# Optimization experiments

Measured on AMD Instinct MI355X. Metric: run time of the kernel, lower is better.

## Reference

```python
import jax, jax.numpy as jnp
import numpy as np

B, T, HW, N, HID, K, OUT = 8, 64, 64, 64, 64, 2, 1
DT = 0.1


def setup_inputs() -> dict:
    key = jax.random.key(0)
    ks = jax.random.split(key, 16)
    nrm = lambda k, shape, s: jax.random.normal(k, shape, jnp.float32) * s
    return {
        "frames": jax.random.uniform(ks[0], (B, T, HW, HW, 3), jnp.float32),
        "adjacency": jax.random.uniform(ks[1], (B, T, N, N), jnp.float32) / N,
        "hidden0": jnp.zeros((B, N, HID), jnp.float32),
        "Wc1": nrm(ks[2], (32, 3, 3, 3), 0.3), "bc1": jnp.zeros(32, jnp.float32),
        "Wc2": nrm(ks[3], (64, 32, 3, 3), 0.08), "bc2": jnp.zeros(64, jnp.float32),
        "Wc3": nrm(ks[4], (128, 64, 3, 3), 0.06), "bc3": jnp.zeros(128, jnp.float32),
        "We": nrm(ks[5], (128, HID), 0.09), "be": jnp.zeros(HID, jnp.float32),
        "Wh": nrm(ks[6], (K + 1, HID, HID), 0.12),
        "Wx": nrm(ks[7], (K + 1, HID, HID), 0.12),
        "bg": jnp.zeros(HID, jnp.float32),
        "tau": jnp.ones(HID, jnp.float32),
        "Ap": nrm(ks[8], (HID,), 1.0),
        "Wd1": nrm(ks[9], (HID, 128), 0.12), "bd1": jnp.zeros(128, jnp.float32),
        "Wd2": nrm(ks[10], (128, 64), 0.09), "bd2": jnp.zeros(64, jnp.float32),
        "Wd3": nrm(ks[11], (64, OUT), 0.12), "bd3": jnp.zeros(OUT, jnp.float32),
    }


def _conv_relu(x, w, b, stride):
    # torch Conv2d(k=3, stride=2, padding=1) == explicit padding (1,1)
    y = jax.lax.conv_general_dilated(
        x, w, (stride, stride), [(1, 1), (1, 1)],
        dimension_numbers=("NCHW", "OIHW", "NCHW"))
    return jax.nn.relu(y + b[None, :, None, None])


def _forward(frames, adjacency, hidden0, Wc1, bc1, Wc2, bc2, Wc3, bc3,
             We, be, Wh, Wx, bg, tau, Ap, Wd1, bd1, Wd2, bd2, Wd3, bd3):
    Bn, Tn, Hh, Ww, C = frames.shape
    # faithful to torch .view(-1, C, H, W): raw memory reinterpretation
    x = frames.reshape(Bn * Tn, C, Hh, Ww)
    x = _conv_relu(x, Wc1, bc1, 2)   # [BT,32,32,32]
    x = _conv_relu(x, Wc2, bc2, 2)   # [BT,64,16,16]
    x = _conv_relu(x, Wc3, bc3, 2)   # [BT,128,8,8]; AdaptiveAvgPool2d((8,8)) is identity here
    feats = x.reshape(Bn, Tn, 128, 8, 8).transpose(0, 1, 3, 4, 2).reshape(Bn, Tn, 64, 128)
    node = feats @ We + be           # [B,T,N,HID]

    Kp = Wh.shape[0] - 1
    eye = jnp.eye(adjacency.shape[-1], dtype=frames.dtype)

    def step(h, inputs):
        xt, At = inputs              # [B,N,HID], [B,N,N]
        powers = [jnp.broadcast_to(eye, At.shape)]
        p = At
        for _ in range(Kp):          # static K-loop -> [I, A, ..., A^K]
            powers.append(p)
            p = jnp.matmul(p, At)
        S = jnp.stack(powers)        # [K+1,B,N,N]
        z = jnp.einsum("bnd,kde->kbne", h, Wh) + jnp.einsum("bnd,kde->kbne", xt, Wx)
        gc = jnp.einsum("kbnm,kbme->bne", S, z) + bg
        f = jnp.tanh(gc)
        h_next = h + DT * (-(1.0 / tau + f) * h + f * Ap)  # liquid time-constant Euler step
        m = h_next.mean(axis=1)      # [B,HID]
        d = jax.nn.relu(m @ Wd1 + bd1)
        d = jax.nn.relu(d @ Wd2 + bd2)
        c = d @ Wd3 + bd3            # [B,OUT]
        return h_next, c

    xs = (node.transpose(1, 0, 2, 3), adjacency.transpose(1, 0, 2, 3))
    final_h, controls = jax.lax.scan(step, hidden0, xs)
    controls = controls.transpose(1, 0, 2)  # [B,T,OUT]
    return controls, final_h


def reference(frames, adjacency, hidden0, Wc1, bc1, Wc2, bc2, Wc3, bc3,
              We, be, Wh, Wx, bg, tau, Ap, Wd1, bd1, Wd2, bd2, Wd3, bd3):
    return _forward(frames, adjacency, hidden0, Wc1, bc1, Wc2, bc2, Wc3, bc3,
                    We, be, Wh, Wx, bg, tau, Ap, Wd1, bd1, Wd2, bd2, Wd3, bd3)
```

## Files before the change

### kernel.cpp

```cpp
#include <hip/hip_runtime.h>
#include <hip/hip_bf16.h>

#define SH 68
#define DT_C 0.1f

typedef short bfrag __attribute__((ext_vector_type(8)));
typedef _Float16 hfrag __attribute__((ext_vector_type(8)));
typedef float f32x4 __attribute__((ext_vector_type(4)));

union FU { bfrag v; unsigned short s[8]; uint4 q; };
union HU { hfrag v; unsigned short s[8]; uint4 q; };

__device__ __forceinline__ unsigned short bf16_rn(float x) {
  union { float f; unsigned u; } v; v.f = x;
  unsigned r = v.u + 0x7fffu + ((v.u >> 16) & 1u);
  return (unsigned short)(r >> 16);
}
__device__ __forceinline__ float bf16_tof(unsigned short h) {
  union { unsigned u; float f; } v; v.u = ((unsigned)h) << 16; return v.f;
}
__device__ __forceinline__ unsigned short bfu(float x) {
  union { __hip_bfloat16 b; unsigned short u; } cv;
  cv.b = __float2bfloat16(x);
  return cv.u;
}
__device__ __forceinline__ float tanh_f(float x) {
  return 1.0f - 2.0f / (__expf(2.0f * x) + 1.0f);
}
__device__ __forceinline__ void h16split(float v, unsigned short& hu, unsigned short& lu) {
  union { _Float16 h; unsigned short u; } a, b;
  a.h = (_Float16)v;
  b.h = (_Float16)(v - (float)a.h);
  hu = a.u; lu = b.u;
}
__device__ __forceinline__ unsigned short h16hi(float v) {
  union { _Float16 h; unsigned short u; } a; a.h = (_Float16)v; return a.u;
}

__device__ __forceinline__ void mm16(const float* __restrict__ A,
                                     const float* __restrict__ B, int sb,
                                     float acc[4][4], int n0, int e0) {
  #pragma unroll 4
  for (int k4 = 0; k4 < 16; ++k4) {
    float4 av0 = *(const float4*)(A + (n0+0)*SH + k4*4);
    float4 av1 = *(const float4*)(A + (n0+1)*SH + k4*4);
    float4 av2 = *(const float4*)(A + (n0+2)*SH + k4*4);
    float4 av3 = *(const float4*)(A + (n0+3)*SH + k4*4);
    const float a0j[4] = {av0.x, av0.y, av0.z, av0.w};
    const float a1j[4] = {av1.x, av1.y, av1.z, av1.w};
    const float a2j[4] = {av2.x, av2.y, av2.z, av2.w};
    const float a3j[4] = {av3.x, av3.y, av3.z, av3.w};
    #pragma unroll
    for (int j = 0; j < 4; ++j) {
      const float4 bv = *(const float4*)(B + (k4*4+j)*sb + e0);
      acc[0][0]+=a0j[j]*bv.x; acc[0][1]+=a0j[j]*bv.y; acc[0][2]+=a0j[j]*bv.z; acc[0][3]+=a0j[j]*bv.w;
      acc[1][0]+=a1j[j]*bv.x; acc[1][1]+=a1j[j]*bv.y; acc[1][2]+=a1j[j]*bv.z; acc[1][3]+=a1j[j]*bv.w;
      acc[2][0]+=a2j[j]*bv.x; acc[2][1]+=a2j[j]*bv.y; acc[2][2]+=a2j[j]*bv.z; acc[2][3]+=a2j[j]*bv.w;
      acc[3][0]+=a3j[j]*bv.x; acc[3][1]+=a3j[j]*bv.y; acc[3][2]+=a3j[j]*bv.z; acc[3][3]+=a3j[j]*bv.w;
    }
  }
}

__global__ __launch_bounds__(256) void wprep_k(const float* __restrict__ Wc2,
                                               const float* __restrict__ Wc3,
                                               const float* __restrict__ Wh,
                                               const float* __restrict__ We,
                                               unsigned short* __restrict__ W2h,
                                               unsigned short* __restrict__ W2l,
                                               unsigned short* __restrict__ W3h,
                                               unsigned short* __restrict__ W3l,
                                               unsigned short* __restrict__ WTh,
                                               unsigned short* __restrict__ WTl,
                                               unsigned short* __restrict__ WeTh,
                                               unsigned short* __restrict__ WeTl) {
  int i = blockIdx.x * 256 + threadIdx.x;
  if (i < 18432) {
    int oc = i / 288, rem = i % 288, pos = rem >> 5, ic = rem & 31;
    float v = Wc2[oc*288 + ic*9 + pos];
    h16split(v, W2h[i], W2l[i]);
  } else if (i < 18432 + 73728) {
    int j = i - 18432;
    int oc = j / 576, rem = j % 576, pos = rem >> 6, ic = rem & 63;
    float v = Wc3[oc*576 + ic*9 + pos];
    h16split(v, W3h[j], W3l[j]);
  } else if (i < 18432 + 73728 + 12288) {
    int j = i - 92160;
    int k3 = j >> 12, rem = j & 4095, din = rem >> 6, dout = rem & 63;
    float v = Wh[j];
    unsigned short hi = bf16_rn(v);
    WTh[k3*4096 + dout*64 + din] = hi;
    WTl[k3*4096 + dout*64 + din] = bf16_rn(v - bf16_tof(hi));
  } else if (i < 18432 + 73728 + 12288 + 8192) {
    int j = i - 104448;
    int e = j >> 7, oc = j & 127;
    float v = We[oc*64 + e];
    h16split(v, WeTh[j], WeTl[j]);
  }
}

__global__ __launch_bounds__(256) void conv1_k(const float* __restrict__ frames,
                                               const float* __restrict__ W,
                                               const float* __restrict__ bias,
                                               unsigned short* __restrict__ c1h) {
  __shared__ __align__(16) float sIn[12288];
  int bt = blockIdx.x, tid = threadIdx.x;
  const float4* src = (const float4*)(frames + (size_t)bt * 12288);
  for (int i = tid; i < 3072; i += 256) ((float4*)sIn)[i] = src[i];
  __syncthreads();
  for (int p = tid; p < 1024; p += 256) {
    int ho = p >> 5, wo = p & 31, hi0 = ho*2-1, wi0 = wo*2-1;
    int obase = (((ho*2 + (wo&1))*16 + (wo>>1)))*8;
    for (int ocb = 0; ocb < 4; ++ocb) {
      float acc[8];
      #pragma unroll
      for (int j = 0; j < 8; ++j) acc[j] = bias[ocb*8+j];
      for (int ic = 0; ic < 3; ++ic) {
        float win[9];
        #pragma unroll
        for (int kh = 0; kh < 3; ++kh) {
          int hi = hi0 + kh;
          #pragma unroll
          for (int kw = 0; kw < 3; ++kw) {
            int wi = wi0 + kw;
            win[kh*3+kw] = (hi>=0 && hi<64 && wi>=0 && wi<64) ? sIn[ic*4096 + hi*64 + wi] : 0.f;
          }
        }
        #pragma unroll
        for (int j = 0; j < 8; ++j) {
          const float* wp = W + (size_t)(ocb*8+j)*27 + ic*9;
          #pragma unroll
          for (int k = 0; k < 9; ++k) acc[j] += win[k] * wp[k];
        }
      }
      ushort hh[8];
      #pragma unroll
      for (int j = 0; j < 8; ++j) hh[j] = h16hi(fmaxf(acc[j], 0.f));
      *(uint4*)&c1h[(size_t)bt*32768 + ocb*8192 + obase] = *(uint4*)hh;
    }
  }
}

#define MFMAH(a, bb, cc) __builtin_amdgcn_mfma_f32_16x16x32_f16((a), (bb), (cc), 0, 0, 0)

__global__ __launch_bounds__(256) void conv2m_k(const unsigned short* __restrict__ c1h,
                                                const unsigned short* __restrict__ W2h,
                                                const unsigned short* __restrict__ W2l,
                                                const float* __restrict__ bias,
                                                unsigned short* __restrict__ c2h) {
  __shared__ __align__(16) unsigned short sH[32768];
  int bt = blockIdx.x, tid = threadIdx.x;
  {
    const uint4* gh = (const uint4*)(c1h + (size_t)bt*32768);
    for (int i = tid; i < 4096; i += 256) ((uint4*)sH)[i] = gh[i];
  }
  __syncthreads();
  int lane = tid & 63, w = tid >> 6, g = lane >> 4, c = lane & 15;
  f32x4 acc[4][4] = {};
  const uint4 z4 = make_uint4(0,0,0,0);
  #pragma unroll
  for (int pos = 0; pos < 9; ++pos) {
    const int kh = pos / 3, kw = pos % 3;
    HU Ah[4];
    #pragma unroll
    for (int m = 0; m < 4; ++m) {
      int pix = w*64 + m*16 + c;
      int ho = pix >> 4, wo = pix & 15;
      int hi = 2*ho - 1 + kh, wi = 2*wo - 1 + kw;
      bool ok = (hi >= 0) & (wi >= 0);
      int hic = ok ? hi : 0, wic = ok ? wi : 0;
      int a = (((g*32 + hic)*2 + (wic & 1))*16 + (wic >> 1))*8;
      uint4 vh = *(const uint4*)&sH[a];
      Ah[m].q = ok ? vh : z4;
    }
    HU Bh[4], Bl[4];
    #pragma unroll
    for (int n = 0; n < 4; ++n) {
      int off = (n*16 + c)*288 + pos*32 + g*8;
      Bh[n].q = *(const uint4*)(W2h + off);
      Bl[n].q = *(const uint4*)(W2l + off);
    }
    #pragma unroll
    for (int m = 0; m < 4; ++m)
      #pragma unroll
      for (int n = 0; n < 4; ++n) {
        acc[m][n] = MFMAH(Ah[m].v, Bh[n].v, acc[m][n]);
        acc[m][n] = MFMAH(Ah[m].v, Bl[n].v, acc[m][n]);
      }
  }
  #pragma unroll
  for (int n = 0; n < 4; ++n) {
    int oc = n*16 + c;
    float bv = bias[oc];
    int ks3 = oc >> 3, il = oc & 7;
    #pragma unroll
    for (int m = 0; m < 4; ++m) {
      #pragma unroll
      for (int r = 0; r < 4; ++r) {
        int pix = w*64 + m*16 + 4*g + r;
        int ho = pix >> 4, wo = pix & 15;
        float v = fmaxf(acc[m][n][r] + bv, 0.f);
        size_t dst = (size_t)bt*16384 + ((((ks3*16 + ho)*2 + (wo&1))*8 + (wo>>1)))*8 + il;
        c2h[dst] = h16hi(v);
      }
    }
  }
}

__global__ __launch_bounds__(256) void conv3e_k(const unsigned short* __restrict__ c2h,
                                                const unsigned short* __restrict__ W3h,
                                                const unsigned short* __restrict__ W3l,
                                                const float* __restrict__ bias,
                                                const unsigned short* __restrict__ WeTh,
                                                const unsigned short* __restrict__ WeTl,
                                                const float* __restrict__ be,
                                                float* __restrict__ node) {
  __shared__ __align__(16) unsigned short sH[16384];
  __shared__ __align__(16) unsigned short sF[64*136];
  int bt = blockIdx.x, tid = threadIdx.x;
  {
    const uint4* gh = (const uint4*)(c2h + (size_t)bt*16384);
    for (int i = tid; i < 2048; i += 256) ((uint4*)sH)[i] = gh[i];
  }
  __syncthreads();
  int lane = tid & 63, w = tid >> 6, g = lane >> 4, c = lane & 15;
  f32x4 acc[8] = {};
  const uint4 z4 = make_uint4(0,0,0,0);
  int pix = w*16 + c;
  int ho = pix >> 3, wo = pix & 7;
  #pragma unroll
  for (int pos = 0; pos < 9; ++pos) {
    const int kh = pos / 3, kw = pos % 3;
    int hi = 2*ho - 1 + kh, wi = 2*wo - 1 + kw;
    bool ok = (hi >= 0) & (wi >= 0);
    int hic = ok ? hi : 0, wic = ok ? wi : 0;
    #pragma unroll
    for (int ih = 0; ih < 2; ++ih) {
      int icg = ih*4 + g;
      int a = ((((icg*16 + hic)*2 + (wic & 1))*8 + (wic >> 1)))*8;
      HU Ah;
      uint4 vh = *(const uint4*)&sH[a];
      Ah.q = ok ? vh : z4;
      #pragma unroll
      for (int n = 0; n < 8; ++n) {
        int off = (n*16 + c)*576 + pos*64 + ih*32 + g*8;
        HU Bh, Bl;
        Bh.q = *(const uint4*)(W3h + off);
        Bl.q = *(const uint4*)(W3l + off);
        acc[n] = MFMAH(Ah.v, Bh.v, acc[n]);
        acc[n] = MFMAH(Ah.v, Bl.v, acc[n]);
      }
    }
  }
  #pragma unroll
  for (int n = 0; n < 8; ++n) {
    int oc = n*16 + c;
    float bv = bias[oc];
    #pragma unroll
    for (int r = 0; r < 4; ++r) {
      int po = w*16 + 4*g + r;
      sF[po*136 + oc] = h16hi(fmaxf(acc[n][r] + bv, 0.f));
    }
  }
  __syncthreads();
  f32x4 eacc[4] = {{0.f,0.f,0.f,0.f},{0.f,0.f,0.f,0.f},{0.f,0.f,0.f,0.f},{0.f,0.f,0.f,0.f}};
  #pragma unroll
  for (int kt = 0; kt < 4; ++kt) {
    HU Af;
    Af.q = *(const uint4*)&sF[(w*16 + c)*136 + kt*32 + g*8];
    #pragma unroll
    for (int n = 0; n < 4; ++n) {
      int off = (n*16 + c)*128 + kt*32 + g*8;
      HU Bh, Bl;
      Bh.q = *(const uint4*)(WeTh + off);
      Bl.q = *(const uint4*)(WeTl + off);
      eacc[n] = MFMAH(Af.v, Bh.v, eacc[n]);
      eacc[n] = MFMAH(Af.v, Bl.v, eacc[n]);
    }
  }
  #pragma unroll
  for (int n = 0; n < 4; ++n) {
    int e = n*16 + c;
    float bev = be[e];
    #pragma unroll
    for (int r = 0; r < 4; ++r) {
      int po = w*16 + 4*g + r;
      node[(size_t)bt*4096 + po*64 + e] = eacc[n][r] + bev;
    }
  }
}

__global__ __launch_bounds__(256) void prep_k(const float* __restrict__ adj,
                                              const float* __restrict__ node,
                                              const float* __restrict__ Wx,
                                              unsigned short* __restrict__ Abf,
                                              unsigned short* __restrict__ A2bf,
                                              float* __restrict__ gxg) {
  __shared__ __align__(16) float sA[64*SH], sA2[64*SH], sN[64*SH], sZ[64*SH];
  int bt = blockIdx.x, tid = threadIdx.x;
  {
    const float4* a4 = (const float4*)(adj + (size_t)bt * 4096);
    const float4* n4 = (const float4*)(node + (size_t)bt * 4096);
    for (int i = tid; i < 1024; i += 256) {
      int r = i >> 4, c = (i & 15) * 4;
      *(float4*)&sA[r*SH+c] = a4[i];
      *(float4*)&sN[r*SH+c] = n4[i];
    }
  }
  __syncthreads();
  int lane = tid & 63, w = tid >> 6, nsub = lane >> 4, eb = lane & 15;
  int n0 = w*16 + nsub*4, e0 = eb*4;
  float4* gxout = (float4*)(gxg + (size_t)bt * 4096);
  for (int i = tid; i < 1024; i += 256) {
    int r = i >> 4, c0 = (i & 15) * 4;
    ushort4 o;
    o.x = bf16_rn(sA[r*SH+c0+0]); o.y = bf16_rn(sA[r*SH+c0+1]);
    o.z = bf16_rn(sA[r*SH+c0+2]); o.w = bf16_rn(sA[r*SH+c0+3]);
    *(ushort4*)&Abf[(size_t)bt*4096 + r*64 + c0] = o;
  }
  {
    float a2t[4][4] = {};
    mm16(sA, sA, SH, a2t, n0, e0);
    #pragma unroll
    for (int jj = 0; jj < 4; ++jj) {
      *(float4*)&sA2[(n0+jj)*SH+e0] = make_float4(a2t[jj][0], a2t[jj][1], a2t[jj][2], a2t[jj][3]);
      ushort4 o;
      o.x = bf16_rn(a2t[jj][0]); o.y = bf16_rn(a2t[jj][1]);
      o.z = bf16_rn(a2t[jj][2]); o.w = bf16_rn(a2t[jj][3]);
      *(ushort4*)&A2bf[(size_t)bt*4096 + (n0+jj)*64 + e0] = o;
    }
  }
  {
    float t[4][4] = {};
    mm16(sN, Wx + 4096, 64, t, n0, e0);
    #pragma unroll
    for (int jj = 0; jj < 4; ++jj)
      *(float4*)&sZ[(n0+jj)*SH+e0] = make_float4(t[jj][0], t[jj][1], t[jj][2], t[jj][3]);
  }
  __syncthreads();
  float gx[4][4] = {};
  mm16(sA, sZ, SH, gx, n0, e0);
  __syncthreads();
  {
    float t[4][4] = {};
    mm16(sN, Wx + 8192, 64, t, n0, e0);
    #pragma unroll
    for (int jj = 0; jj < 4; ++jj)
      *(float4*)&sZ[(n0+jj)*SH+e0] = make_float4(t[jj][0], t[jj][1], t[jj][2], t[jj][3]);
  }
  __syncthreads();
  mm16(sA2, sZ, SH, gx, n0, e0);
  mm16(sN, Wx, 64, gx, n0, e0);
  #pragma unroll
  for (int jj = 0; jj < 4; ++jj)
    gxout[(n0+jj)*16 + eb] = make_float4(gx[jj][0], gx[jj][1], gx[jj][2], gx[jj][3]);
}

#define MFMA(a, bb, cc) __builtin_amdgcn_mfma_f32_16x16x32_bf16((a), (bb), (cc), 0, 0, 0)

__global__ __launch_bounds__(1024, 4) void seq2_k(
    const unsigned short* __restrict__ Abf, const unsigned short* __restrict__ A2bf,
    const float* __restrict__ gxg, const float* __restrict__ h0,
    const unsigned short* __restrict__ WTh, const unsigned short* __restrict__ WTl,
    const float* __restrict__ bg, const float* __restrict__ tau, const float* __restrict__ Apv,
    float* __restrict__ mout, float* __restrict__ out) {
  __shared__ unsigned short sHh[64*72];
  __shared__ unsigned short sA[2][64*72], sA2[2][64*72];
  __shared__ unsigned short sZ1[64*72], sZ2[64*72];
  __shared__ float sPart[64*17];
  int b = blockIdx.x, tid = threadIdx.x;
  int lane = tid & 63, w = tid >> 6, g = lane >> 4, c = lane & 15;
  int mt = w & 3, nt = w >> 2;
  int e = nt*16 + c;
  int mrow = mt*16 + 4*g;
  float itau = 1.f/tau[e], apv = Apv[e], bgv = bg[e];
  FU wf[3][2][2];
  #pragma unroll
  for (int k3 = 0; k3 < 3; ++k3)
    #pragma unroll
    for (int kt = 0; kt < 2; ++kt) {
      int off = k3*4096 + e*64 + kt*32 + 8*g;
      wf[k3][kt][0].q = *(const uint4*)(WTh + off);
      wf[k3][kt][1].q = *(const uint4*)(WTl + off);
    }
  float hm[4];
  #pragma unroll
  for (int r = 0; r < 4; ++r) hm[r] = h0[(size_t)b*4096 + (mrow+r)*64 + e];
  #pragma unroll
  for (int r = 0; r < 4; ++r) sHh[(mrow+r)*72 + e] = bfu(hm[r]);
  {
    int row = tid >> 4, k0 = (tid & 15) * 4;
    *(uint2*)&sA[0][row*72 + k0]  = *(const uint2*)(Abf  + (size_t)b*64*4096 + tid*4);
    *(uint2*)&sA2[0][row*72 + k0] = *(const uint2*)(A2bf + (size_t)b*64*4096 + tid*4);
  }
  __syncthreads();
  #pragma unroll 1
  for (int t = 0; t < 64; ++t) {
    int cur = t & 1;
    size_t bt = (size_t)b*64 + t;
    int tn = (t < 63) ? t + 1 : t;
    uint2 pa  = *(const uint2*)(Abf  + ((size_t)b*64 + tn)*4096 + tid*4);
    uint2 pa2 = *(const uint2*)(A2bf + ((size_t)b*64 + tn)*4096 + tid*4);
    float gxv[4];
    {
      const float* gp = gxg + bt*4096;
      #pragma unroll
      for (int r = 0; r < 4; ++r) gxv[r] = gp[(mrow+r)*64 + e];
    }
    FU ha[2];
    #pragma unroll
    for (int kt = 0; kt < 2; ++kt)
      ha[kt].q = *(const uint4*)&sHh[(mt*16 + c)*72 + kt*32 + 8*g];
    f32x4 a1 = {0.f,0.f,0.f,0.f}, a2 = {0.f,0.f,0.f,0.f};
    #pragma unroll
    for (int kt = 0; kt < 2; ++kt) {
      a1 = MFMA(ha[kt].v, wf[1][kt][0].v, a1);
      a1 = MFMA(ha[kt].v, wf[1][kt][1].v, a1);
      a2 = MFMA(ha[kt].v, wf[2][kt][0].v, a2);
      a2 = MFMA(ha[kt].v, wf[2][kt][1].v, a2);
    }
    {
      ushort4 o1, o2;
      o1.x = bfu(a1[0]); o1.y = bfu(a1[1]); o1.z = bfu(a1[2]); o1.w = bfu(a1[3]);
      o2.x = bfu(a2[0]); o2.y = bfu(a2[1]); o2.z = bfu(a2[2]); o2.w = bfu(a2[3]);
      *(ushort4*)&sZ1[e*72 + mrow] = o1;
      *(ushort4*)&sZ2[e*72 + mrow] = o2;
    }
    __syncthreads();
    f32x4 acc = {0.f,0.f,0.f,0.f};
    #pragma unroll
    for (int kt = 0; kt < 2; ++kt) {
      FU aA, aA2, z1f, z2f;
      int ao = (mt*16 + c)*72 + kt*32 + 8*g;
      aA.q  = *(const uint4*)&sA[cur][ao];
      aA2.q = *(const uint4*)&sA2[cur][ao];
      z1f.q = *(const uint4*)&sZ1[e*72 + kt*32 + 8*g];
      z2f.q = *(const uint4*)&sZ2[e*72 + kt*32 + 8*g];
      acc = MFMA(ha[kt].v, wf[0][kt][0].v, acc);
      acc = MFMA(ha[kt].v, wf[0][kt][1].v, acc);
      acc = MFMA(aA.v,  z1f.v, acc);
      acc = MFMA(aA2.v, z2f.v, acc);
    }
    float ps = 0.f;
    #pragma unroll
    for (int r = 0; r < 4; ++r) {
      float gc = acc[r] + gxv[r] + bgv;
      float f = tanh_f(gc);
      float hn = hm[r] + DT_C * (-(itau + f) * hm[r] + f * apv);
      hm[r] = hn;
      ps += hn;
      sHh[(mrow+r)*72 + e] = bfu(hn);
    }
    sPart[e*17 + mt*4 + g] = ps;
    {
      int row = tid >> 4, k0 = (tid & 15) * 4;
      *(uint2*)&sA[cur^1][row*72 + k0]  = pa;
      *(uint2*)&sA2[cur^1][row*72 + k0] = pa2;
    }
    __syncthreads();
    if (lane < 4) {
      int ee = w*4 + lane;
      float s = 0.f;
      #pragma unroll
      for (int j = 0; j < 16; ++j) s += sPart[ee*17 + j];
      mout[bt*64 + ee] = s * (1.0f / 64.0f);
    }
  }
  #pragma unroll
  for (int r = 0; r < 4; ++r)
    out[512 + (size_t)b*4096 + (mrow+r)*64 + e] = hm[r];
}

__global__ __launch_bounds__(128) void dec_k(const float* __restrict__ mout,
                                             const float* __restrict__ Wd1, const float* __restrict__ bd1,
                                             const float* __restrict__ Wd2, const float* __restrict__ bd2,
                                             const float* __restrict__ Wd3, const float* __restrict__ bd3,
                                             float* __restrict__ out) {
  __shared__ float sm[64], sd1[128], sd2[64];
  int bt = blockIdx.x, tid = threadIdx.x;
  if (tid < 64) sm[tid] = mout[(size_t)bt*64 + tid];
  __syncthreads();
  {
    float a = bd1[tid];
    #pragma unroll 8
    for (int e = 0; e < 64; ++e) a += sm[e] * Wd1[e*128 + tid];
    sd1[tid] = fmaxf(a, 0.f);
  }
  __syncthreads();
  if (tid < 64) {
    float a = bd2[tid];
    #pragma unroll 8
    for (int i = 0; i < 128; ++i) a += sd1[i] * Wd2[i*64 + tid];
    sd2[tid] = fmaxf(a, 0.f);
  }
  __syncthreads();
  if (tid < 64) {
    float p = sd2[tid] * Wd3[tid];
    #pragma unroll
    for (int off = 32; off > 0; off >>= 1) p += __shfl_down(p, off, 64);
    if (tid == 0) out[bt] = p + bd3[0];
  }
}

extern "C" void kernel_launch(void* const* d_in, const int* in_sizes, int n_in,
                              void* d_out, int out_size, void* d_ws, size_t ws_size,
                              hipStream_t stream) {
  const float* frames = (const float*)d_in[0];
  const float* adj    = (const float*)d_in[1];
  const float* h0     = (const float*)d_in[2];
  const float* Wc1 = (const float*)d_in[3];  const float* bc1 = (const float*)d_in[4];
  const float* Wc2 = (const float*)d_in[5];  const float* bc2 = (const float*)d_in[6];
  const float* Wc3 = (const float*)d_in[7];  const float* bc3 = (const float*)d_in[8];
  const float* We  = (const float*)d_in[9];  const float* be  = (const float*)d_in[10];
  const float* Wh  = (const float*)d_in[11]; const float* Wx  = (const float*)d_in[12];
  const float* bg  = (const float*)d_in[13]; const float* tau = (const float*)d_in[14];
  const float* Ap  = (const float*)d_in[15];
  const float* Wd1 = (const float*)d_in[16]; const float* bd1 = (const float*)d_in[17];
  const float* Wd2 = (const float*)d_in[18]; const float* bd2 = (const float*)d_in[19];
  const float* Wd3 = (const float*)d_in[20]; const float* bd3 = (const float*)d_in[21];

  float* ws = (float*)d_ws;
  unsigned short* c1h = (unsigned short*)(ws);
  unsigned short* c2h = (unsigned short*)(ws + 16777216);
  unsigned short* W2h = (unsigned short*)(ws + 20971520);
  unsigned short* W2l = (unsigned short*)(ws + 20980736);
  unsigned short* W3h = (unsigned short*)(ws + 20989952);
  unsigned short* W3l = (unsigned short*)(ws + 21026816);
  unsigned short* WTh = (unsigned short*)(ws + 21063680);
  unsigned short* WTl = (unsigned short*)(ws + 21069824);
  unsigned short* WeTh = (unsigned short*)(ws + 21075968);
  unsigned short* WeTl = (unsigned short*)(ws + 21080064);
  float* node = ws + 4194304;
  float* gx   = ws + 6291456;
  unsigned short* Abf  = (unsigned short*)(ws + 8388608);
  unsigned short* A2bf = (unsigned short*)(ws + 9437184);
  float* mo   = ws + 10485760;
  float* out  = (float*)d_out;

  wprep_k <<<440, 256, 0, stream>>>(Wc2, Wc3, Wh, We, W2h, W2l, W3h, W3l, WTh, WTl, WeTh, WeTl);
  conv1_k <<<512, 256, 0, stream>>>(frames, Wc1, bc1, c1h);
  conv2m_k<<<512, 256, 0, stream>>>(c1h, W2h, W2l, bc2, c2h);
  conv3e_k<<<512, 256, 0, stream>>>(c2h, W3h, W3l, bc3, WeTh, WeTl, be, node);
  prep_k  <<<512, 256, 0, stream>>>(adj, node, Wx, Abf, A2bf, gx);
  seq2_k  <<<8,  1024, 0, stream>>>(Abf, A2bf, gx, h0, WTh, WTl, bg, tau, Ap, mo, out);
  dec_k   <<<512, 128, 0, stream>>>(mo, Wd1, bd1, Wd2, bd2, Wd3, bd3, out);
}
```

Before: 302.2 us.

## Move adjacency-precompute kernel from FP32 FMA to split-bf16 MFMA

Replaces the scalar FP32 prep kernel (A^2, node@Wx terms, and gx accumulation) with an MFMA-based version that splits operands into bf16 hi/lo pairs and uses three MFMAs per product to keep near-FP32 accuracy. Wx is pre-transposed and split in the weight-prep kernel, and the block grows to 512 threads. This targets the per-timestep prep cost that runs before the sequential scan, in exchange for extra split/convert work and more shared-memory traffic.

After: 293.4 us. 1.03x faster.

```diff
diff --git a/kernel.cpp b/kernel.cpp
--- a/kernel.cpp
+++ b/kernel.cpp
@@ -1,8 +1,8 @@
 #include <hip/hip_runtime.h>
 #include <hip/hip_bf16.h>
 
-#define SH 68
 #define DT_C 0.1f
+#define PS 72
 
 typedef short bfrag __attribute__((ext_vector_type(8)));
 typedef _Float16 hfrag __attribute__((ext_vector_type(8)));
@@ -37,34 +37,11 @@
   union { _Float16 h; unsigned short u; } a; a.h = (_Float16)v; return a.u;
 }
 
-__device__ __forceinline__ void mm16(const float* __restrict__ A,
-                                     const float* __restrict__ B, int sb,
-                                     float acc[4][4], int n0, int e0) {
-  #pragma unroll 4
-  for (int k4 = 0; k4 < 16; ++k4) {
-    float4 av0 = *(const float4*)(A + (n0+0)*SH + k4*4);
-    float4 av1 = *(const float4*)(A + (n0+1)*SH + k4*4);
-    float4 av2 = *(const float4*)(A + (n0+2)*SH + k4*4);
-    float4 av3 = *(const float4*)(A + (n0+3)*SH + k4*4);
-    const float a0j[4] = {av0.x, av0.y, av0.z, av0.w};
-    const float a1j[4] = {av1.x, av1.y, av1.z, av1.w};
-    const float a2j[4] = {av2.x, av2.y, av2.z, av2.w};
-    const float a3j[4] = {av3.x, av3.y, av3.z, av3.w};
-    #pragma unroll
-    for (int j = 0; j < 4; ++j) {
-      const float4 bv = *(const float4*)(B + (k4*4+j)*sb + e0);
-      acc[0][0]+=a0j[j]*bv.x; acc[0][1]+=a0j[j]*bv.y; acc[0][2]+=a0j[j]*bv.z; acc[0][3]+=a0j[j]*bv.w;
-      acc[1][0]+=a1j[j]*bv.x; acc[1][1]+=a1j[j]*bv.y; acc[1][2]+=a1j[j]*bv.z; acc[1][3]+=a1j[j]*bv.w;
-      acc[2][0]+=a2j[j]*bv.x; acc[2][1]+=a2j[j]*bv.y; acc[2][2]+=a2j[j]*bv.z; acc[2][3]+=a2j[j]*bv.w;
-      acc[3][0]+=a3j[j]*bv.x; acc[3][1]+=a3j[j]*bv.y; acc[3][2]+=a3j[j]*bv.z; acc[3][3]+=a3j[j]*bv.w;
-    }
-  }
-}
-
 __global__ __launch_bounds__(256) void wprep_k(const float* __restrict__ Wc2,
                                                const float* __restrict__ Wc3,
                                                const float* __restrict__ Wh,
                                                const float* __restrict__ We,
+                                               const float* __restrict__ Wx,
                                                unsigned short* __restrict__ W2h,
                                                unsigned short* __restrict__ W2l,
                                                unsigned short* __restrict__ W3h,
@@ -72,29 +49,38 @@
                                                unsigned short* __restrict__ WTh,
                                                unsigned short* __restrict__ WTl,
                                                unsigned short* __restrict__ WeTh,
-                                               unsigned short* __restrict__ WeTl) {
+                                               unsigned short* __restrict__ WeTl,
+                                               unsigned short* __restrict__ WxTh,
+                                               unsigned short* __restrict__ WxTl) {
   int i = blockIdx.x * 256 + threadIdx.x;
   if (i < 18432) {
     int oc = i / 288, rem = i % 288, pos = rem >> 5, ic = rem & 31;
     float v = Wc2[oc*288 + ic*9 + pos];
     h16split(v, W2h[i], W2l[i]);
-  } else if (i < 18432 + 73728) {
+  } else if (i < 92160) {
     int j = i - 18432;
     int oc = j / 576, rem = j % 576, pos = rem >> 6, ic = rem & 63;
     float v = Wc3[oc*576 + ic*9 + pos];
     h16split(v, W3h[j], W3l[j]);
-  } else if (i < 18432 + 73728 + 12288) {
+  } else if (i < 104448) {
     int j = i - 92160;
     int k3 = j >> 12, rem = j & 4095, din = rem >> 6, dout = rem & 63;
     float v = Wh[j];
     unsigned short hi = bf16_rn(v);
     WTh[k3*4096 + dout*64 + din] = hi;
     WTl[k3*4096 + dout*64 + din] = bf16_rn(v - bf16_tof(hi));
-  } else if (i < 18432 + 73728 + 12288 + 8192) {
+  } else if (i < 112640) {
     int j = i - 104448;
     int e = j >> 7, oc = j & 127;
     float v = We[oc*64 + e];
     h16split(v, WeTh[j], WeTl[j]);
+  } else if (i < 124928) {
+    int j = i - 112640;
+    int k3 = j >> 12, rem = j & 4095, e = rem >> 6, din = rem & 63;
+    float v = Wx[k3*4096 + din*64 + e];
+    unsigned short hi = bf16_rn(v);
+    WxTh[j] = hi;
+    WxTl[j] = bf16_rn(v - bf16_tof(hi));
   }
 }
 
@@ -289,73 +275,172 @@
   }
 }
 
-__global__ __launch_bounds__(256) void prep_k(const float* __restrict__ adj,
-                                              const float* __restrict__ node,
-                                              const float* __restrict__ Wx,
-                                              unsigned short* __restrict__ Abf,
-                                              unsigned short* __restrict__ A2bf,
-                                              float* __restrict__ gxg) {
-  __shared__ __align__(16) float sA[64*SH], sA2[64*SH], sN[64*SH], sZ[64*SH];
+#define MFMA(a, bb, cc) __builtin_amdgcn_mfma_f32_16x16x32_bf16((a), (bb), (cc), 0, 0, 0)
+
+__global__ __launch_bounds__(512) void prepm_k(const float* __restrict__ adj,
+                                               const float* __restrict__ node,
+                                               const unsigned short* __restrict__ WxTh,
+                                               const unsigned short* __restrict__ WxTl,
+                                               unsigned short* __restrict__ Abf,
+                                               unsigned short* __restrict__ A2bf,
+                                               float* __restrict__ gxg) {
+  __shared__ __align__(16) unsigned short sAh[64*PS], sAl[64*PS];
+  __shared__ __align__(16) unsigned short sXh[64*PS], sXl[64*PS];
+  __shared__ __align__(16) unsigned short sNh[64*PS], sNl[64*PS];
+  __shared__ __align__(16) unsigned short sZh[64*PS], sZl[64*PS];
   int bt = blockIdx.x, tid = threadIdx.x;
-  {
-    const float4* a4 = (const float4*)(adj + (size_t)bt * 4096);
-    const float4* n4 = (const float4*)(node + (size_t)bt * 4096);
-    for (int i = tid; i < 1024; i += 256) {
-      int r = i >> 4, c = (i & 15) * 4;
-      *(float4*)&sA[r*SH+c] = a4[i];
-      *(float4*)&sN[r*SH+c] = n4[i];
-    }
-  }
-  __syncthreads();
-  int lane = tid & 63, w = tid >> 6, nsub = lane >> 4, eb = lane & 15;
-  int n0 = w*16 + nsub*4, e0 = eb*4;
-  float4* gxout = (float4*)(gxg + (size_t)bt * 4096);
-  for (int i = tid; i < 1024; i += 256) {
+  int lane = tid & 63, w = tid >> 6, g = lane >> 4, c = lane & 15;
+  int mt = w & 3, nt0 = (w >> 2) * 2;
+  int mrow = mt*16 + 4*g;
+  for (int i = tid; i < 1024; i += 512) {
     int r = i >> 4, c0 = (i & 15) * 4;
-    ushort4 o;
-    o.x = bf16_rn(sA[r*SH+c0+0]); o.y = bf16_rn(sA[r*SH+c0+1]);
-    o.z = bf16_rn(sA[r*SH+c0+2]); o.w = bf16_rn(sA[r*SH+c0+3]);
-    *(ushort4*)&Abf[(size_t)bt*4096 + r*64 + c0] = o;
-  }
-  {
-    float a2t[4][4] = {};
-    mm16(sA, sA, SH, a2t, n0, e0);
-    #pragma unroll
-    for (int jj = 0; jj < 4; ++jj) {
-      *(float4*)&sA2[(n0+jj)*SH+e0] = make_float4(a2t[jj][0], a2t[jj][1], a2t[jj][2], a2t[jj][3]);
-      ushort4 o;
-      o.x = bf16_rn(a2t[jj][0]); o.y = bf16_rn(a2t[jj][1]);
-      o.z = bf16_rn(a2t[jj][2]); o.w = bf16_rn(a2t[jj][3]);
-      *(ushort4*)&A2bf[(size_t)bt*4096 + (n0+jj)*64 + e0] = o;
-    }
-  }
-  {
-    float t[4][4] = {};
-    mm16(sN, Wx + 4096, 64, t, n0, e0);
-    #pragma unroll
-    for (int jj = 0; jj < 4; ++jj)
-      *(float4*)&sZ[(n0+jj)*SH+e0] = make_float4(t[jj][0], t[jj][1], t[jj][2], t[jj][3]);
-  }
-  __syncthreads();
-  float gx[4][4] = {};
-  mm16(sA, sZ, SH, gx, n0, e0);
-  __syncthreads();
-  {
-    float t[4][4] = {};
-    mm16(sN, Wx + 8192, 64, t, n0, e0);
-    #pragma unroll
-    for (int jj = 0; jj < 4; ++jj)
-      *(float4*)&sZ[(n0+jj)*SH+e0] = make_float4(t[jj][0], t[jj][1], t[jj][2], t[jj][3]);
-  }
-  __syncthreads();
-  mm16(sA2, sZ, SH, gx, n0, e0);
-  mm16(sN, Wx, 64, gx, n0, e0);
-  #pragma unroll
-  for (int jj = 0; jj < 4; ++jj)
-    gxout[(n0+jj)*16 + eb] = make_float4(gx[jj][0], gx[jj][1], gx[jj][2], gx[jj][3]);
-}
-
-#define MFMA(a, bb, cc) __builtin_amdgcn_mfma_f32_16x16x32_bf16((a), (bb), (cc), 0, 0, 0)
+    float4 av = ((const float4*)(adj + (size_t)bt*4096))[i];
+    float4 nv = ((const float4*)(node + (size_t)bt*4096))[i];
+    float aa[4] = {av.x, av.y, av.z, av.w};
+    float nn[4] = {nv.x, nv.y, nv.z, nv.w};
+    ushort4 ah4, al4, nh4, nl4;
+    #pragma unroll
+    for (int j = 0; j < 4; ++j) {
+      unsigned short hi = bf16_rn(aa[j]);
+      unsigned short lo = bf16_rn(aa[j] - bf16_tof(hi));
+      ((unsigned short*)&ah4)[j] = hi;
+      ((unsigned short*)&al4)[j] = lo;
+      sXh[(c0+j)*PS + r] = hi;
+      sXl[(c0+j)*PS + r] = lo;
+      unsigned short nhi = bf16_rn(nn[j]);
+      ((unsigned short*)&nh4)[j] = nhi;
+      ((unsigned short*)&nl4)[j] = bf16_rn(nn[j] - bf16_tof(nhi));
+    }
+    *(ushort4*)&sAh[r*PS + c0] = ah4;
+    *(ushort4*)&sAl[r*PS + c0] = al4;
+    *(ushort4*)&sNh[r*PS + c0] = nh4;
+    *(ushort4*)&sNl[r*PS + c0] = nl4;
+    *(ushort4*)&Abf[(size_t)bt*4096 + r*64 + c0] = ah4;
+  }
+  __syncthreads();
+  FU a_h[2], a_l[2], n_h[2], n_l[2];
+  #pragma unroll
+  for (int kt = 0; kt < 2; ++kt) {
+    int ao = (mt*16 + c)*PS + kt*32 + 8*g;
+    a_h[kt].q = *(const uint4*)&sAh[ao];
+    a_l[kt].q = *(const uint4*)&sAl[ao];
+    n_h[kt].q = *(const uint4*)&sNh[ao];
+    n_l[kt].q = *(const uint4*)&sNl[ao];
+  }
+  f32x4 a2f[2] = {{0.f,0.f,0.f,0.f},{0.f,0.f,0.f,0.f}};
+  f32x4 zf[2]  = {{0.f,0.f,0.f,0.f},{0.f,0.f,0.f,0.f}};
+  #pragma unroll
+  for (int tt = 0; tt < 2; ++tt) {
+    int e = (nt0+tt)*16 + c;
+    #pragma unroll
+    for (int kt = 0; kt < 2; ++kt) {
+      FU bh, bl;
+      int bo = e*PS + kt*32 + 8*g;
+      bh.q = *(const uint4*)&sXh[bo];
+      bl.q = *(const uint4*)&sXl[bo];
+      a2f[tt] = MFMA(a_h[kt].v, bh.v, a2f[tt]);
+      a2f[tt] = MFMA(a_l[kt].v, bh.v, a2f[tt]);
+      a2f[tt] = MFMA(a_h[kt].v, bl.v, a2f[tt]);
+      FU wh, wl;
+      int wo = 4096 + e*64 + kt*32 + 8*g;
+      wh.q = *(const uint4*)(WxTh + wo);
+      wl.q = *(const uint4*)(WxTl + wo);
+      zf[tt] = MFMA(n_h[kt].v, wh.v, zf[tt]);
+      zf[tt] = MFMA(n_l[kt].v, wh.v, zf[tt]);
+      zf[tt] = MFMA(n_h[kt].v, wl.v, zf[tt]);
+    }
+  }
+  __syncthreads();
+  #pragma unroll
+  for (int tt = 0; tt < 2; ++tt) {
+    int e = (nt0+tt)*16 + c;
+    ushort4 zh4, zl4;
+    #pragma unroll
+    for (int r = 0; r < 4; ++r) {
+      float va = a2f[tt][r];
+      unsigned short ahi = bf16_rn(va);
+      sXh[(mrow+r)*PS + e] = ahi;
+      sXl[(mrow+r)*PS + e] = bf16_rn(va - bf16_tof(ahi));
+      A2bf[(size_t)bt*4096 + (mrow+r)*64 + e] = ahi;
+      float vz = zf[tt][r];
+      unsigned short zhi = bf16_rn(vz);
+      ((unsigned short*)&zh4)[r] = zhi;
+      ((unsigned short*)&zl4)[r] = bf16_rn(vz - bf16_tof(zhi));
+    }
+    *(ushort4*)&sZh[e*PS + mrow] = zh4;
+    *(ushort4*)&sZl[e*PS + mrow] = zl4;
+  }
+  __syncthreads();
+  f32x4 gacc[2] = {{0.f,0.f,0.f,0.f},{0.f,0.f,0.f,0.f}};
+  #pragma unroll
+  for (int tt = 0; tt < 2; ++tt) {
+    int e = (nt0+tt)*16 + c;
+    zf[tt][0] = 0.f; zf[tt][1] = 0.f; zf[tt][2] = 0.f; zf[tt][3] = 0.f;
+    #pragma unroll
+    for (int kt = 0; kt < 2; ++kt) {
+      FU bh, bl;
+      int bo = e*PS + kt*32 + 8*g;
+      bh.q = *(const uint4*)&sZh[bo];
+      bl.q = *(const uint4*)&sZl[bo];
+      gacc[tt] = MFMA(a_h[kt].v, bh.v, gacc[tt]);
+      gacc[tt] = MFMA(a_l[kt].v, bh.v, gacc[tt]);
+      gacc[tt] = MFMA(a_h[kt].v, bl.v, gacc[tt]);
+      FU wh, wl;
+      int w0 = e*64 + kt*32 + 8*g;
+      wh.q = *(const uint4*)(WxTh + w0);
+      wl.q = *(const uint4*)(WxTl + w0);
+      gacc[tt] = MFMA(n_h[kt].v, wh.v, gacc[tt]);
+      gacc[tt] = MFMA(n_l[kt].v, wh.v, gacc[tt]);
+      gacc[tt] = MFMA(n_h[kt].v, wl.v, gacc[tt]);
+      int w2 = 8192 + e*64 + kt*32 + 8*g;
+      wh.q = *(const uint4*)(WxTh + w2);
+      wl.q = *(const uint4*)(WxTl + w2);
+      zf[tt] = MFMA(n_h[kt].v, wh.v, zf[tt]);
+      zf[tt] = MFMA(n_l[kt].v, wh.v, zf[tt]);
+      zf[tt] = MFMA(n_h[kt].v, wl.v, zf[tt]);
+    }
+  }
+  __syncthreads();
+  #pragma unroll
+  for (int tt = 0; tt < 2; ++tt) {
+    int e = (nt0+tt)*16 + c;
+    ushort4 zh4, zl4;
+    #pragma unroll
+    for (int r = 0; r < 4; ++r) {
+      float vz = zf[tt][r];
+      unsigned short zhi = bf16_rn(vz);
+      ((unsigned short*)&zh4)[r] = zhi;
+      ((unsigned short*)&zl4)[r] = bf16_rn(vz - bf16_tof(zhi));
+    }
+    *(ushort4*)&sZh[e*PS + mrow] = zh4;
+    *(ushort4*)&sZl[e*PS + mrow] = zl4;
+  }
+  __syncthreads();
+  FU p_h[2], p_l[2];
+  #pragma unroll
+  for (int kt = 0; kt < 2; ++kt) {
+    int po = (mt*16 + c)*PS + kt*32 + 8*g;
+    p_h[kt].q = *(const uint4*)&sXh[po];
+    p_l[kt].q = *(const uint4*)&sXl[po];
+  }
+  #pragma unroll
+  for (int tt = 0; tt < 2; ++tt) {
+    int e = (nt0+tt)*16 + c;
+    #pragma unroll
+    for (int kt = 0; kt < 2; ++kt) {
+      FU bh, bl;
+      int bo = e*PS + kt*32 + 8*g;
+      bh.q = *(const uint4*)&sZh[bo];
+      bl.q = *(const uint4*)&sZl[bo];
+      gacc[tt] = MFMA(p_h[kt].v, bh.v, gacc[tt]);
+      gacc[tt] = MFMA(p_l[kt].v, bh.v, gacc[tt]);
+      gacc[tt] = MFMA(p_h[kt].v, bl.v, gacc[tt]);
+    }
+    #pragma unroll
+    for (int r = 0; r < 4; ++r)
+      gxg[(size_t)bt*4096 + (mrow+r)*64 + e] = gacc[tt][r];
+  }
+}
 
 __global__ __launch_bounds__(1024, 4) void seq2_k(
     const unsigned short* __restrict__ Abf, const unsigned short* __restrict__ A2bf,
@@ -529,6 +614,8 @@
   unsigned short* WTl = (unsigned short*)(ws + 21069824);
   unsigned short* WeTh = (unsigned short*)(ws + 21075968);
   unsigned short* WeTl = (unsigned short*)(ws + 21080064);
+  unsigned short* WxTh = (unsigned short*)(ws + 21084160);
+  unsigned short* WxTl = (unsigned short*)(ws + 21090304);
   float* node = ws + 4194304;
   float* gx   = ws + 6291456;
   unsigned short* Abf  = (unsigned short*)(ws + 8388608);
@@ -536,11 +623,12 @@
   float* mo   = ws + 10485760;
   float* out  = (float*)d_out;
 
-  wprep_k <<<440, 256, 0, stream>>>(Wc2, Wc3, Wh, We, W2h, W2l, W3h, W3l, WTh, WTl, WeTh, WeTl);
+  wprep_k <<<488, 256, 0, stream>>>(Wc2, Wc3, Wh, We, Wx, W2h, W2l, W3h, W3l,
+                                    WTh, WTl, WeTh, WeTl, WxTh, WxTl);
   conv1_k <<<512, 256, 0, stream>>>(frames, Wc1, bc1, c1h);
   conv2m_k<<<512, 256, 0, stream>>>(c1h, W2h, W2l, bc2, c2h);
   conv3e_k<<<512, 256, 0, stream>>>(c2h, W3h, W3l, bc3, WeTh, WeTl, be, node);
-  prep_k  <<<512, 256, 0, stream>>>(adj, node, Wx, Abf, A2bf, gx);
+  prepm_k <<<512, 512, 0, stream>>>(adj, node, WxTh, WxTl, Abf, A2bf, gx);
   seq2_k  <<<8,  1024, 0, stream>>>(Abf, A2bf, gx, h0, WTh, WTl, bg, tau, Ap, mo, out);
   dec_k   <<<512, 128, 0, stream>>>(mo, Wd1, bd1, Wd2, bd2, Wd3, bd3, out);
 }
```
